# Optimization experiments

Hardware: AMD Instinct MI355X
Metric: run time of the kernel (lower is better)

The kernel has to match this reference:

```python
import jax, jax.numpy as jnp
import numpy as np

D = 4096          # in = out features of the quantized linear
K = 128           # n_quantize (codebook size)
B, S = 4, 4096    # batch, seq_len


def setup_inputs() -> dict:
    key = jax.random.key(0)
    k1, k2, k3, k4 = jax.random.split(key, 4)
    x = jax.random.normal(k1, (B, S, D), dtype=jnp.float32)
    quantized_vectors = jax.random.normal(k2, (D, K), dtype=jnp.float32)
    assignments = jax.random.randint(k3, (D,), 0, K, dtype=jnp.int32)
    bias = jax.random.normal(k4, (D,), dtype=jnp.float32)
    return {"x": x, "quantized_vectors": quantized_vectors,
            "assignments": assignments, "bias": bias}


def reference(x, quantized_vectors, assignments, bias):
    orig_shape = x.shape
    x_flat = x.reshape(-1, quantized_vectors.shape[0])          # [T, D]
    # row-gather the codebook then skinny matmul: [T, D] @ [D, K] -> [T, K]
    gathered = jnp.take(quantized_vectors, assignments, axis=0)  # [D, K]
    qm = jnp.einsum('ij,jk->ik', x_flat, gathered)               # [T, K]
    # column gather back to D outputs, add bias
    out = jnp.take(qm, assignments, axis=1) + bias[None, :]      # [T, D]
    return out.reshape(orig_shape)
```

## Files before the change

kernel.cpp:

```cpp
#include <hip/hip_runtime.h>
#include <hip/hip_fp16.h>

#define DD 4096
#define KK 128
#define MAXHC 48
#define XL2 4112
#define QVC_OFF 24832

union H2 { unsigned int u; __half2 h; };

static __device__ __forceinline__ unsigned int pkh2(float lo, float hi) {
    H2 r; r.h = __floats2half2_rn(lo, hi); return r.u;
}

__global__ void vq_build(const float* __restrict__ qv,
                         const int* __restrict__ assign,
                         unsigned short* __restrict__ perm2,
                         int* __restrict__ maxh,
                         float4* __restrict__ qvC) {
    const int tid = threadIdx.x;

    if (blockIdx.x == 1) {
        for (int idx = tid; idx < 4096; idx += 256) {
            const int c4 = idx >> 7;
            const int k  = idx & (KK - 1);
            float4 v;
            v.x = qv[(4 * c4 + 0) * KK + k];
            v.y = qv[(4 * c4 + 1) * KK + k];
            v.z = qv[(4 * c4 + 2) * KK + k];
            v.w = qv[(4 * c4 + 3) * KK + k];
            qvC[idx] = v;
        }
        return;
    }

    __shared__ int cnt[KK];
    __shared__ int off[KK];

    if (tid < KK) cnt[tid] = 0;
    for (int i = tid; i < MAXHC * 256; i += 256)
        perm2[i] = (unsigned short)DD;
    __syncthreads();

    for (int j = tid; j < DD; j += 256)
        atomicAdd(&cnt[assign[j]], 1);
    __syncthreads();

    if (tid == 0) {
        int m = 0;
        for (int c = 0; c < KK; ++c) {
            off[c] = 0;
            int h = (cnt[c] + 1) >> 1;
            if (h > m) m = h;
        }
        *maxh = (m < MAXHC) ? m : MAXHC;
    }
    __syncthreads();

    for (int j = tid; j < DD; j += 256) {
        const int c = assign[j];
        const int p = atomicAdd(&off[c], 1);
        const int i = p >> 1;
        const int th = 2 * c + (p & 1);
        if (i < MAXHC)
            perm2[(i >> 1) * 512 + th * 2 + (i & 1)] = (unsigned short)j;
    }
}

__global__ __launch_bounds__(256) void vq_main(
    const float* __restrict__ x,
    const int*   __restrict__ assign,
    const float* __restrict__ bias,
    const unsigned int* __restrict__ pu,
    const int* __restrict__ maxh,
    const float4* __restrict__ qvC,
    float* __restrict__ out)
{
    __shared__ unsigned int xp[2 * XL2];
    __shared__ float xs[4 * KK];
    __shared__ float4 qm4[KK];

    const int t0  = blockIdx.x * 4;
    const int tid = threadIdx.x;

    {
        const float4* r0 = reinterpret_cast<const float4*>(x + (size_t)(t0 + 0) * DD);
        const float4* r1 = reinterpret_cast<const float4*>(x + (size_t)(t0 + 1) * DD);
        const float4* r2 = reinterpret_cast<const float4*>(x + (size_t)(t0 + 2) * DD);
        const float4* r3 = reinterpret_cast<const float4*>(x + (size_t)(t0 + 3) * DD);
        uint4* pa = reinterpret_cast<uint4*>(xp);
        uint4* pb = reinterpret_cast<uint4*>(xp + XL2);
        #pragma unroll
        for (int i = 0; i < 4; ++i) {
            const int idx = tid + i * 256;
            const float4 a = r0[idx];
            const float4 b = r1[idx];
            const float4 c = r2[idx];
            const float4 d = r3[idx];
            uint4 wa, wb;
            wa.x = pkh2(a.x, b.x); wa.y = pkh2(a.y, b.y);
            wa.z = pkh2(a.z, b.z); wa.w = pkh2(a.w, b.w);
            wb.x = pkh2(c.x, d.x); wb.y = pkh2(c.y, d.y);
            wb.z = pkh2(c.z, d.z); wb.w = pkh2(c.w, d.w);
            pa[idx] = wa;
            pb[idx] = wb;
        }
        if (tid == 0) { xp[DD] = 0u; xp[XL2 + DD] = 0u; }
    }
    __syncthreads();

    {
        const int mh2 = (*maxh + 1) >> 1;
        float s0 = 0.f, s1 = 0.f, s2 = 0.f, s3 = 0.f;
        for (int ii = 0; ii < mh2; ++ii) {
            const unsigned int pp = pu[ii * 256 + tid];
            const int i0 = pp & 0xFFFFu;
            const int i1 = pp >> 16;
            H2 wa0, wb0, wa1, wb1;
            wa0.u = xp[i0];        wb0.u = xp[XL2 + i0];
            wa1.u = xp[i1];        wb1.u = xp[XL2 + i1];
            s0 += __low2float(wa0.h);  s1 += __high2float(wa0.h);
            s2 += __low2float(wb0.h);  s3 += __high2float(wb0.h);
            s0 += __low2float(wa1.h);  s1 += __high2float(wa1.h);
            s2 += __low2float(wb1.h);  s3 += __high2float(wb1.h);
        }
        s0 += __shfl_xor(s0, 1);
        s1 += __shfl_xor(s1, 1);
        s2 += __shfl_xor(s2, 1);
        s3 += __shfl_xor(s3, 1);
        if ((tid & 1) == 0) {
            const int c = tid >> 1;
            xs[c]          = s0;
            xs[KK + c]     = s1;
            xs[2 * KK + c] = s2;
            xs[3 * KK + c] = s3;
        }
    }
    __syncthreads();

    {
        const int k = tid >> 1;
        const int h = tid & 1;
        const float4* xsf4 = reinterpret_cast<const float4*>(xs);
        float4 acc[4];
        acc[0] = acc[1] = acc[2] = acc[3] = make_float4(0.f, 0.f, 0.f, 0.f);
        #pragma unroll 4
        for (int c4 = 0; c4 < 16; ++c4) {
            const int cg = h * 16 + c4;
            const float4 q = qvC[cg * KK + k];
            #pragma unroll
            for (int tt = 0; tt < 4; ++tt) {
                const float4 v = xsf4[tt * 32 + cg];
                acc[tt].x += q.x * v.x;
                acc[tt].y += q.y * v.y;
                acc[tt].z += q.z * v.z;
                acc[tt].w += q.w * v.w;
            }
        }
        float r0 = (acc[0].x + acc[0].y) + (acc[0].z + acc[0].w);
        float r1 = (acc[1].x + acc[1].y) + (acc[1].z + acc[1].w);
        float r2 = (acc[2].x + acc[2].y) + (acc[2].z + acc[2].w);
        float r3 = (acc[3].x + acc[3].y) + (acc[3].z + acc[3].w);
        r0 += __shfl_xor(r0, 1);
        r1 += __shfl_xor(r1, 1);
        r2 += __shfl_xor(r2, 1);
        r3 += __shfl_xor(r3, 1);
        if (h == 0) qm4[k] = make_float4(r0, r1, r2, r3);
    }
    __syncthreads();

    {
        const int4*   a4 = reinterpret_cast<const int4*>(assign);
        const float4* b4 = reinterpret_cast<const float4*>(bias);
        float4* o0 = reinterpret_cast<float4*>(out + (size_t)(t0 + 0) * DD);
        float4* o1 = reinterpret_cast<float4*>(out + (size_t)(t0 + 1) * DD);
        float4* o2 = reinterpret_cast<float4*>(out + (size_t)(t0 + 2) * DD);
        float4* o3 = reinterpret_cast<float4*>(out + (size_t)(t0 + 3) * DD);
        #pragma unroll
        for (int i = 0; i < 4; ++i) {
            const int idx = tid + i * 256;
            const int4   a = a4[idx];
            const float4 b = b4[idx];
            const float4 qx = qm4[a.x];
            const float4 qy = qm4[a.y];
            const float4 qz = qm4[a.z];
            const float4 qw = qm4[a.w];
            float4 s;
            s.x = qx.x + b.x; s.y = qy.x + b.y; s.z = qz.x + b.z; s.w = qw.x + b.w;
            o0[idx] = s;
            s.x = qx.y + b.x; s.y = qy.y + b.y; s.z = qz.y + b.z; s.w = qw.y + b.w;
            o1[idx] = s;
            s.x = qx.z + b.x; s.y = qy.z + b.y; s.z = qz.z + b.z; s.w = qw.z + b.w;
            o2[idx] = s;
            s.x = qx.w + b.x; s.y = qy.w + b.y; s.z = qz.w + b.z; s.w = qw.w + b.w;
            o3[idx] = s;
        }
    }
}

extern "C" void kernel_launch(void* const* d_in, const int* in_sizes, int n_in,
                              void* d_out, int out_size, void* d_ws, size_t ws_size,
                              hipStream_t stream) {
    const float* x      = (const float*)d_in[0];
    const float* qv     = (const float*)d_in[1];
    const int*   assign = (const int*)d_in[2];
    const float* bias   = (const float*)d_in[3];
    float*       out    = (float*)d_out;

    unsigned short* perm2 = (unsigned short*)d_ws;
    int*    maxh = (int*)((char*)d_ws + MAXHC * 256 * sizeof(unsigned short));
    float4* qvC  = (float4*)((char*)d_ws + QVC_OFF);

    const int T = in_sizes[0] / DD;

    vq_build<<<dim3(2), dim3(256), 0, stream>>>(qv, assign, perm2, maxh, qvC);
    vq_main<<<dim3(T / 4), dim3(256), 0, stream>>>(
        x, assign, bias, (const unsigned int*)perm2, maxh, qvC, out);
}
```

Measured before the change: 461.7 us.

## Split fused kernel into separate qm-compute and scatter kernels with output-buffer stash

Splits the single fused kernel into two launches. The first reads x, computes the 4x128 qm tile and stashes it in the first 2KB of each block's output rows. The second reloads the stash and writes the full gathered output plus bias. The intent is to separate the read-heavy phase from the write-heavy phase so each kernel has simpler resource use and its memory traffic streams more cleanly. The cost is an extra launch and a small extra write and read of qm through global memory, and it relies on all stashes being read before they are overwritten.

Result: slower. 474.8 us (+2.8%).

```diff
diff --git a/kernel.cpp b/kernel.cpp
--- a/kernel.cpp
+++ b/kernel.cpp
@@ -67,10 +67,8 @@
     }
 }
 
-__global__ __launch_bounds__(256) void vq_main(
+__global__ __launch_bounds__(256) void vq_qm(
     const float* __restrict__ x,
-    const int*   __restrict__ assign,
-    const float* __restrict__ bias,
     const unsigned int* __restrict__ pu,
     const int* __restrict__ maxh,
     const float4* __restrict__ qvC,
@@ -78,7 +76,6 @@
 {
     __shared__ unsigned int xp[2 * XL2];
     __shared__ float xs[4 * KK];
-    __shared__ float4 qm4[KK];
 
     const int t0  = blockIdx.x * 4;
     const int tid = threadIdx.x;
@@ -165,36 +162,60 @@
         r1 += __shfl_xor(r1, 1);
         r2 += __shfl_xor(r2, 1);
         r3 += __shfl_xor(r3, 1);
-        if (h == 0) qm4[k] = make_float4(r0, r1, r2, r3);
-    }
-    __syncthreads();
-
-    {
-        const int4*   a4 = reinterpret_cast<const int4*>(assign);
-        const float4* b4 = reinterpret_cast<const float4*>(bias);
-        float4* o0 = reinterpret_cast<float4*>(out + (size_t)(t0 + 0) * DD);
-        float4* o1 = reinterpret_cast<float4*>(out + (size_t)(t0 + 1) * DD);
-        float4* o2 = reinterpret_cast<float4*>(out + (size_t)(t0 + 2) * DD);
-        float4* o3 = reinterpret_cast<float4*>(out + (size_t)(t0 + 3) * DD);
-        #pragma unroll
-        for (int i = 0; i < 4; ++i) {
-            const int idx = tid + i * 256;
-            const int4   a = a4[idx];
-            const float4 b = b4[idx];
-            const float4 qx = qm4[a.x];
-            const float4 qy = qm4[a.y];
-            const float4 qz = qm4[a.z];
-            const float4 qw = qm4[a.w];
-            float4 s;
-            s.x = qx.x + b.x; s.y = qy.x + b.y; s.z = qz.x + b.z; s.w = qw.x + b.w;
-            o0[idx] = s;
-            s.x = qx.y + b.x; s.y = qy.y + b.y; s.z = qz.y + b.z; s.w = qw.y + b.w;
-            o1[idx] = s;
-            s.x = qx.z + b.x; s.y = qy.z + b.y; s.z = qz.z + b.z; s.w = qw.z + b.w;
-            o2[idx] = s;
-            s.x = qx.w + b.x; s.y = qy.w + b.y; s.z = qz.w + b.z; s.w = qw.w + b.w;
-            o3[idx] = s;
-        }
+        if (h == 0) {
+            float4* stash = reinterpret_cast<float4*>(out + (size_t)t0 * DD);
+            stash[k] = make_float4(r0, r1, r2, r3);
+        }
+    }
+}
+
+__global__ __launch_bounds__(256) void vq_scatter(
+    const int*   __restrict__ assign,
+    const float* __restrict__ bias,
+    float* __restrict__ out)
+{
+    __shared__ float4 qm4[KK];
+
+    const int t0  = blockIdx.x * 4;
+    const int tid = threadIdx.x;
+
+    float4 qs;
+    const float4* stash = reinterpret_cast<const float4*>(out + (size_t)t0 * DD);
+    if (tid < KK) qs = stash[tid];
+
+    const int4*   a4 = reinterpret_cast<const int4*>(assign);
+    const float4* b4 = reinterpret_cast<const float4*>(bias);
+    int4   a[4];
+    float4 b[4];
+    #pragma unroll
+    for (int i = 0; i < 4; ++i) {
+        a[i] = a4[tid + i * 256];
+        b[i] = b4[tid + i * 256];
+    }
+
+    if (tid < KK) qm4[tid] = qs;
+    __syncthreads();
+
+    float4* o0 = reinterpret_cast<float4*>(out + (size_t)(t0 + 0) * DD);
+    float4* o1 = reinterpret_cast<float4*>(out + (size_t)(t0 + 1) * DD);
+    float4* o2 = reinterpret_cast<float4*>(out + (size_t)(t0 + 2) * DD);
+    float4* o3 = reinterpret_cast<float4*>(out + (size_t)(t0 + 3) * DD);
+    #pragma unroll
+    for (int i = 0; i < 4; ++i) {
+        const int idx = tid + i * 256;
+        const float4 qx = qm4[a[i].x];
+        const float4 qy = qm4[a[i].y];
+        const float4 qz = qm4[a[i].z];
+        const float4 qw = qm4[a[i].w];
+        float4 s;
+        s.x = qx.x + b[i].x; s.y = qy.x + b[i].y; s.z = qz.x + b[i].z; s.w = qw.x + b[i].w;
+        o0[idx] = s;
+        s.x = qx.y + b[i].x; s.y = qy.y + b[i].y; s.z = qz.y + b[i].z; s.w = qw.y + b[i].w;
+        o1[idx] = s;
+        s.x = qx.z + b[i].x; s.y = qy.z + b[i].y; s.z = qz.z + b[i].z; s.w = qw.z + b[i].w;
+        o2[idx] = s;
+        s.x = qx.w + b[i].x; s.y = qy.w + b[i].y; s.z = qz.w + b[i].z; s.w = qw.w + b[i].w;
+        o3[idx] = s;
     }
 }
 
@@ -214,6 +235,7 @@
     const int T = in_sizes[0] / DD;
 
     vq_build<<<dim3(2), dim3(256), 0, stream>>>(qv, assign, perm2, maxh, qvC);
-    vq_main<<<dim3(T / 4), dim3(256), 0, stream>>>(
-        x, assign, bias, (const unsigned int*)perm2, maxh, qvC, out);
-}
+    vq_qm<<<dim3(T / 4), dim3(256), 0, stream>>>(
+        x, (const unsigned int*)perm2, maxh, qvC, out);
+    vq_scatter<<<dim3(T / 4), dim3(256), 0, stream>>>(assign, bias, out);
+}
```
